# Kernel tuning notes

Hardware: AMD Instinct MI355X
Metric: run time of the kernel (lower is better)

Reference implementation:

```python
import jax, jax.numpy as jnp
import numpy as np

NUM_EXPERTS = 16  # init_kwargs


def setup_inputs() -> dict:
    key = jax.random.key(0)
    k1, k2, k3 = jax.random.split(key, 3)
    T, D = 8192, 1024
    inp = jax.random.normal(k1, (T, D), dtype=jnp.float32)
    domain_ids = jax.random.randint(k2, (T,), 0, NUM_EXPERTS, dtype=jnp.int32)
    mask = jax.random.bernoulli(k3, 0.1, (T,))
    return {"input": inp, "domain_ids": domain_ids, "mask": mask}


def reference(input, domain_ids, mask):
    T = input.shape[0]
    E = NUM_EXPERTS
    capacity = -(-T // E)  # math.ceil(num_tokens / num_experts)

    # one_hot(domain_ids, num_experts) -> [T, E] (integer, as in torch util)
    mask1 = jax.nn.one_hot(domain_ids, E, dtype=jnp.int32)
    # zero out padded tokens: mask1 * (~mask)
    mask1 = mask1 * (~mask)[:, None].astype(jnp.int32)

    # fused_cumsum_sub_one: cumsum over token dim minus 1 -> position within expert
    locations1 = jnp.cumsum(mask1, axis=0) - 1  # [T, E]

    # drop tokens beyond expert capacity
    mask1 = mask1 * (locations1 < capacity).astype(jnp.int32)

    # capacity slot index for each token (0 where dropped)
    locations1_s = jnp.sum(locations1 * mask1, axis=1)  # [T]

    # gates1_s = ones -> gates1 = mask1 as float
    gates1 = mask1.astype(input.dtype)  # [T, E]

    # one_hot over capacity slots, [T, C]
    loc_sc = jax.nn.one_hot(locations1_s, capacity, dtype=input.dtype)

    # bmm([T,E,1], [T,1,C]) == batched outer product -> [T, E, C]
    combine1_sec = gates1[:, :, None] * loc_sc[:, None, :]
    dispatch_mask = combine1_sec.astype(bool)

    l_aux = jnp.zeros((), dtype=input.dtype)
    return (l_aux, combine1_sec, dispatch_mask)
```

## Files before the change

### kernel.cpp

```cpp
#include <hip/hip_runtime.h>
#include <hip/hip_bf16.h>


#define T_TOKENS 8192
#define NUM_EXPERTS 16
#define CAPACITY 512
#define TEC (67108864ull)
#define TOTAL (134217729ull)

__global__ __launch_bounds__(64)
void DomainGate_scatter(const int* __restrict__ domain_ids,
                        const int* __restrict__ mask_i32,
                        float* __restrict__ out) {
    const int e = blockIdx.x;
    const int lane = threadIdx.x;
    const unsigned long long lane_lt = (lane == 0) ? 0ull : ((1ull << lane) - 1ull);

    int running = 0;
    for (int c = 0; c < T_TOKENS / 256; ++c) {
        const int t0 = c * 256 + lane * 4;
        const int4 e4 = *(const int4*)&domain_ids[t0];
        const int4 m4 = *(const int4*)&mask_i32[t0];

        const int b0 = (e4.x == e) && !m4.x;
        const int b1 = (e4.y == e) && !m4.y;
        const int b2 = (e4.z == e) && !m4.z;
        const int b3 = (e4.w == e) && !m4.w;

        const unsigned long long B0 = __ballot(b0);
        const unsigned long long B1 = __ballot(b1);
        const unsigned long long B2 = __ballot(b2);
        const unsigned long long B3 = __ballot(b3);

        const int before = __popcll(B0 & lane_lt) + __popcll(B1 & lane_lt) +
                           __popcll(B2 & lane_lt) + __popcll(B3 & lane_lt);
        const int r0 = running + before;
        const int r1 = r0 + b0;
        const int r2 = r1 + b1;
        const int r3 = r2 + b2;

        if (b0 && r0 < CAPACITY) {
            const size_t idx = 1ull + ((size_t)(t0 + 0) * NUM_EXPERTS + e) * CAPACITY + (size_t)r0;
            out[idx] = 1.0f; out[idx + TEC] = 1.0f;
        }
        if (b1 && r1 < CAPACITY) {
            const size_t idx = 1ull + ((size_t)(t0 + 1) * NUM_EXPERTS + e) * CAPACITY + (size_t)r1;
            out[idx] = 1.0f; out[idx + TEC] = 1.0f;
        }
        if (b2 && r2 < CAPACITY) {
            const size_t idx = 1ull + ((size_t)(t0 + 2) * NUM_EXPERTS + e) * CAPACITY + (size_t)r2;
            out[idx] = 1.0f; out[idx + TEC] = 1.0f;
        }
        if (b3 && r3 < CAPACITY) {
            const size_t idx = 1ull + ((size_t)(t0 + 3) * NUM_EXPERTS + e) * CAPACITY + (size_t)r3;
            out[idx] = 1.0f; out[idx + TEC] = 1.0f;
        }

        running += __popcll(B0) + __popcll(B1) + __popcll(B2) + __popcll(B3);
    }
}

extern "C" void kernel_launch(void* const* d_in, const int* in_sizes, int n_in,
                              void* d_out, int out_size, void* d_ws, size_t ws_size,
                              hipStream_t stream) {
    (void)in_sizes; (void)n_in; (void)d_ws; (void)ws_size;
    const int* domain_ids = (const int*)d_in[1];
    const int* mask_i32 = (const int*)d_in[2];
    float* out = (float*)d_out;

    hipMemsetAsync(out, 0, (size_t)out_size * sizeof(float), stream);

    DomainGate_scatter<<<NUM_EXPERTS, 64, 0, stream>>>(domain_ids, mask_i32, out);
}
```

Before: 557.7 us.

## Fuse output zeroing with one-hot scatter via precomputed per-row slot table

Replaces the hipMemset plus a 16-block scatter kernel with two kernels. A single-block prep kernel computes each (token, expert) row's capacity slot, or -1, into workspace. A 2048-block fill kernel then zeroes its 256KB chunk with float4 stores and writes the 1.0 entries for rows overlapping that chunk. This removes a separate memset pass and the poorly parallel scatter. It adds a workspace dependency and an intra-block ordering between the zero stores and the scattered stores.

```diff
diff --git a/kernel.cpp b/kernel.cpp
--- a/kernel.cpp
+++ b/kernel.cpp
@@ -5,15 +5,17 @@
 #define T_TOKENS 8192
 #define NUM_EXPERTS 16
 #define CAPACITY 512
-#define TEC (67108864ull)
-#define TOTAL (134217729ull)
+#define TEC (67108864ll)
+#define TOTAL (134217729ll)
+#define NROWS (131072)
+#define FPB (65536ll)
 
-__global__ __launch_bounds__(64)
-void DomainGate_scatter(const int* __restrict__ domain_ids,
-                        const int* __restrict__ mask_i32,
-                        float* __restrict__ out) {
-    const int e = blockIdx.x;
-    const int lane = threadIdx.x;
+__global__ __launch_bounds__(1024)
+void DomainGate_prep(const int* __restrict__ domain_ids,
+                     const int* __restrict__ mask_i32,
+                     int* __restrict__ rowinfo ) {
+    const int wave = threadIdx.x >> 6;
+    const int lane = threadIdx.x & 63;
     const unsigned long long lane_lt = (lane == 0) ? 0ull : ((1ull << lane) - 1ull);
 
     int running = 0;
@@ -22,10 +24,10 @@
         const int4 e4 = *(const int4*)&domain_ids[t0];
         const int4 m4 = *(const int4*)&mask_i32[t0];
 
-        const int b0 = (e4.x == e) && !m4.x;
-        const int b1 = (e4.y == e) && !m4.y;
-        const int b2 = (e4.z == e) && !m4.z;
-        const int b3 = (e4.w == e) && !m4.w;
+        const int b0 = (e4.x == wave) && !m4.x;
+        const int b1 = (e4.y == wave) && !m4.y;
+        const int b2 = (e4.z == wave) && !m4.z;
+        const int b3 = (e4.w == wave) && !m4.w;
 
         const unsigned long long B0 = __ballot(b0);
         const unsigned long long B1 = __ballot(b1);
@@ -39,36 +41,62 @@
         const int r2 = r1 + b1;
         const int r3 = r2 + b2;
 
-        if (b0 && r0 < CAPACITY) {
-            const size_t idx = 1ull + ((size_t)(t0 + 0) * NUM_EXPERTS + e) * CAPACITY + (size_t)r0;
-            out[idx] = 1.0f; out[idx + TEC] = 1.0f;
-        }
-        if (b1 && r1 < CAPACITY) {
-            const size_t idx = 1ull + ((size_t)(t0 + 1) * NUM_EXPERTS + e) * CAPACITY + (size_t)r1;
-            out[idx] = 1.0f; out[idx + TEC] = 1.0f;
-        }
-        if (b2 && r2 < CAPACITY) {
-            const size_t idx = 1ull + ((size_t)(t0 + 2) * NUM_EXPERTS + e) * CAPACITY + (size_t)r2;
-            out[idx] = 1.0f; out[idx + TEC] = 1.0f;
-        }
-        if (b3 && r3 < CAPACITY) {
-            const size_t idx = 1ull + ((size_t)(t0 + 3) * NUM_EXPERTS + e) * CAPACITY + (size_t)r3;
-            out[idx] = 1.0f; out[idx + TEC] = 1.0f;
-        }
+        int4 o;
+        o.x = (b0 && r0 < CAPACITY) ? r0 : -1;
+        o.y = (b1 && r1 < CAPACITY) ? r1 : -1;
+        o.z = (b2 && r2 < CAPACITY) ? r2 : -1;
+        o.w = (b3 && r3 < CAPACITY) ? r3 : -1;
+        *(int4*)&rowinfo[wave * T_TOKENS + t0] = o;
 
         running += __popcll(B0) + __popcll(B1) + __popcll(B2) + __popcll(B3);
+    }
+}
+
+__global__ __launch_bounds__(256)
+void DomainGate_fill(const int* __restrict__ rowinfo, float* __restrict__ out) {
+    const long long f0 = (long long)blockIdx.x * FPB;
+    long long f1 = f0 + FPB;
+    if (blockIdx.x == gridDim.x - 1) f1 = TOTAL;
+
+    {
+        float4* p = (float4*)(out + f0);
+        const float4 z = make_float4(0.f, 0.f, 0.f, 0.f);
+        #pragma unroll 8
+        for (int i = 0; i < (int)(FPB / 4 / 256); ++i)
+            p[i * 256 + threadIdx.x] = z;
+        if (f1 != f0 + FPB && threadIdx.x == 0)
+            out[TOTAL - 1] = 0.0f;
+    }
+    __syncthreads();
+
+    #pragma unroll
+    for (int h = 0; h < 2; ++h) {
+        const long long base = 1ll + (long long)h * TEC;
+        long long lo = (f0 - base) >> 9;
+        if (lo < 0) lo = 0;
+        long long hi = (f1 - 1 - base) >> 9;
+        if (hi >= NROWS) hi = NROWS - 1;
+        const long long r = lo + (long long)threadIdx.x;
+        if (r <= hi) {
+            const int row = (int)r;
+            const int op = rowinfo[((row & 15) << 13) | (row >> 4)];
+            if (op >= 0) {
+                const long long idx = base + ((long long)row << 9) + op;
+                if (idx >= f0 && idx < f1) out[idx] = 1.0f;
+            }
+        }
     }
 }
 
 extern "C" void kernel_launch(void* const* d_in, const int* in_sizes, int n_in,
                               void* d_out, int out_size, void* d_ws, size_t ws_size,
                               hipStream_t stream) {
-    (void)in_sizes; (void)n_in; (void)d_ws; (void)ws_size;
+    (void)in_sizes; (void)n_in; (void)out_size; (void)ws_size;
     const int* domain_ids = (const int*)d_in[1];
     const int* mask_i32 = (const int*)d_in[2];
     float* out = (float*)d_out;
+    int* rowinfo = (int*)d_ws;
 
-    hipMemsetAsync(out, 0, (size_t)out_size * sizeof(float), stream);
-
-    DomainGate_scatter<<<NUM_EXPERTS, 64, 0, stream>>>(domain_ids, mask_i32, out);
+    DomainGate_prep<<<1, 1024, 0, stream>>>(domain_ids, mask_i32, rowinfo);
+    DomainGate_fill<<<2048, 256, 0, stream>>>(rowinfo, out);
 }
```

Measured after the change: 556.3 us. No clear change (-0.2%).
